# Kernel tuning notes

Hardware: AMD Instinct MI355X
Metric: run time of the kernel (lower is better)

## Reference

```python
import jax, jax.numpy as jnp
import numpy as np

N = 100_000   # nodes
E = 1_000_000 # edges
F = 128       # nfeat
H = 2         # heads
C = 64        # nhid (per-head out channels)
NEG_SLOPE = 0.2
BN_EPS = 1e-5


def setup_inputs() -> dict:
    key = jax.random.key(0)
    ks = jax.random.split(key, 6)
    x = jax.random.normal(ks[0], (N, F), dtype=jnp.float32)
    edge_index = jax.random.randint(ks[1], (2, E), 0, N, dtype=jnp.int32)
    # GATConv params (xavier-ish scale)
    W = jax.random.normal(ks[2], (F, H * C), dtype=jnp.float32) * np.float32(1.0 / np.sqrt(F))
    att_src = jax.random.normal(ks[3], (H, C), dtype=jnp.float32) * np.float32(0.1)
    att_dst = jax.random.normal(ks[4], (H, C), dtype=jnp.float32) * np.float32(0.1)
    bias = jnp.zeros((H * C,), dtype=jnp.float32)
    # BatchNorm1d affine params
    gamma = jnp.ones((H * C,), dtype=jnp.float32)
    beta = jnp.zeros((H * C,), dtype=jnp.float32)
    return {"x": x, "edge_index": edge_index, "W": W, "att_src": att_src,
            "att_dst": att_dst, "bias": bias, "gamma": gamma, "beta": beta}


def reference(x, edge_index, W, att_src, att_dst, bias, gamma, beta):
    n = x.shape[0]
    # --- GATConv (PyG semantics): add self-loops, per-head linear, edge attention ---
    loop = jnp.arange(n, dtype=edge_index.dtype)
    src = jnp.concatenate([edge_index[0], loop])  # message sources (j)
    dst = jnp.concatenate([edge_index[1], loop])  # aggregation targets (i)

    h = (x @ W).reshape(n, H, C)                      # [N,H,C]
    a_src = jnp.einsum('nhc,hc->nh', h, att_src)      # [N,H]
    a_dst = jnp.einsum('nhc,hc->nh', h, att_dst)      # [N,H]

    e = jax.nn.leaky_relu(a_src[src] + a_dst[dst], NEG_SLOPE)  # [Et,H]
    # segment softmax over incoming edges of each dst node
    m = jax.lax.stop_gradient(jax.ops.segment_max(e, dst, num_segments=n))
    e = jnp.exp(e - m[dst])
    s = jax.ops.segment_sum(e, dst, num_segments=n)
    alpha = e / s[dst]                                 # [Et,H]

    out = jax.ops.segment_sum(alpha[:, :, None] * h[src], dst, num_segments=n)  # [N,H,C]
    out = out.reshape(n, H * C) + bias                 # concat heads + bias

    # --- transition: ReLU -> BatchNorm1d (training-mode batch stats) -> Dropout(eval=identity) ---
    out = jax.nn.relu(out)
    mean = out.mean(axis=0)
    var = out.var(axis=0)  # biased, as BN uses for normalization
    out = gamma * (out - mean) * jax.lax.rsqrt(var + BN_EPS) + beta
    return out
```

## Files before the change

### kernel.cpp

```cpp
#include <hip/hip_runtime.h>

#define NN 100000
#define EE 1000000
#define ET (EE + NN)
#define HC 128
#define NB 391
#define AGG_BLOCKS 2048
#define NGRP (NN / 4)
#define NTILE 6250

typedef __attribute__((ext_vector_type(8))) short short8;
typedef __attribute__((ext_vector_type(4))) float f32x4;

__device__ __forceinline__ unsigned bfpack(float a, float b) {
    unsigned ua = __float_as_uint(a), ub = __float_as_uint(b);
    ua += 0x7fff + ((ua >> 16) & 1);
    ub += 0x7fff + ((ub >> 16) & 1);
    return (ua >> 16) | (ub & 0xffff0000u);
}

__global__ __launch_bounds__(64) void k_wprep(const float* __restrict__ W,
                                              uint4* __restrict__ wf)
{
    const int bid = blockIdx.x;
    const int ks = bid >> 3, nt = bid & 7;
    const int l = threadIdx.x;
    const int n = nt * 16 + (l & 15);
    const int k0 = ks * 32 + (l >> 4) * 8;
    unsigned u[4];
    #pragma unroll
    for (int r = 0; r < 4; ++r)
        u[r] = bfpack(W[(k0 + 2*r) * HC + n], W[(k0 + 2*r + 1) * HC + n]);
    wf[bid * 64 + l] = make_uint4(u[0], u[1], u[2], u[3]);
}

__global__ __launch_bounds__(256) void k_gemm(
    const float* __restrict__ x, const uint4* __restrict__ wf,
    const float* __restrict__ atts, const float* __restrict__ attd,
    unsigned* __restrict__ hB, float2* __restrict__ asrc2, float2* __restrict__ adst2)
{
    __shared__ uint4 wl[2048];
    for (int i = threadIdx.x; i < 2048; i += 256) wl[i] = wf[i];
    __syncthreads();

    const int wv = threadIdx.x >> 6, lane = threadIdx.x & 63;
    const int g = lane >> 4, c15 = lane & 15;

    float As[8], Ad[8];
    #pragma unroll
    for (int nt = 0; nt < 8; ++nt) {
        As[nt] = atts[nt * 16 + c15];
        Ad[nt] = attd[nt * 16 + c15];
    }

    for (int t = blockIdx.x * 4 + wv; t < NTILE; t += gridDim.x * 4) {
        const int row0 = t * 16;
        union { unsigned u[4]; short8 v; } af[4];
        const float* xr = x + (size_t)(row0 + c15) * HC + g * 8;
        #pragma unroll
        for (int ks = 0; ks < 4; ++ks) {
            float4 lo = *(const float4*)(xr + ks * 32);
            float4 hi = *(const float4*)(xr + ks * 32 + 4);
            af[ks].u[0] = bfpack(lo.x, lo.y);
            af[ks].u[1] = bfpack(lo.z, lo.w);
            af[ks].u[2] = bfpack(hi.x, hi.y);
            af[ks].u[3] = bfpack(hi.z, hi.w);
        }
        f32x4 acc[8];
        #pragma unroll
        for (int nt = 0; nt < 8; ++nt) acc[nt] = (f32x4)(0.f);
        #pragma unroll
        for (int nt = 0; nt < 8; ++nt) {
            #pragma unroll
            for (int ks = 0; ks < 4; ++ks) {
                short8 bfr = *(const short8*)&wl[(ks * 8 + nt) * 64 + lane];
                acc[nt] = __builtin_amdgcn_mfma_f32_16x16x32_bf16(
                    af[ks].v, bfr, acc[nt], 0, 0, 0);
            }
        }
        #pragma unroll
        for (int r = 0; r < 4; ++r) {
            const int row = row0 + g * 4 + r;
            float ps = 0.f, pd = 0.f, qs = 0.f, qd = 0.f;
            #pragma unroll
            for (int nt = 0; nt < 4; ++nt) {
                float a = acc[nt][r], b = acc[nt + 4][r];
                hB[(size_t)row * 64 + nt * 16 + c15] = bfpack(a, b);
                ps += a * As[nt];     qs += a * Ad[nt];
                pd += b * As[nt + 4]; qd += b * Ad[nt + 4];
            }
            for (int off = 8; off; off >>= 1) {
                ps += __shfl_xor(ps, off); pd += __shfl_xor(pd, off);
                qs += __shfl_xor(qs, off); qd += __shfl_xor(qd, off);
            }
            if (c15 == 0) {
                asrc2[row] = make_float2(ps, pd);
                adst2[row] = make_float2(qs, qd);
            }
        }
    }
}

__device__ __forceinline__ void edge_sd(const int* __restrict__ ei, int t, int& s, int& d) {
    if (t < EE) { s = ei[t]; d = ei[EE + t]; }
    else        { s = t - EE; d = t - EE; }
}

__global__ __launch_bounds__(256) void k_hist(const int* __restrict__ ei,
                                              int* __restrict__ hist)
{
    int t = blockIdx.x * 256 + threadIdx.x;
    if (t >= ET) return;
    int d = (t < EE) ? ei[EE + t] : (t - EE);
    atomicAdd(&hist[d], 1);
}

__global__ __launch_bounds__(256) void k_scan1(const int* __restrict__ hist,
                                               int* __restrict__ part)
{
    __shared__ int ls[256];
    int i = blockIdx.x * 256 + threadIdx.x;
    ls[threadIdx.x] = (i < NN) ? hist[i] : 0;
    __syncthreads();
    for (int off = 128; off; off >>= 1) {
        if (threadIdx.x < off) ls[threadIdx.x] += ls[threadIdx.x + off];
        __syncthreads();
    }
    if (!threadIdx.x) part[blockIdx.x] = ls[0];
}

__global__ __launch_bounds__(512) void k_scan2(int* __restrict__ part)
{
    __shared__ int ls[512];
    int tid = threadIdx.x;
    int v = (tid < NB) ? part[tid] : 0;
    ls[tid] = v;
    __syncthreads();
    for (int off = 1; off < 512; off <<= 1) {
        int t = (tid >= off) ? ls[tid - off] : 0;
        __syncthreads();
        ls[tid] += t;
        __syncthreads();
    }
    if (tid < NB) part[tid] = ls[tid] - v;
}

__global__ __launch_bounds__(256) void k_scan3(const int* __restrict__ hist,
                                               const int* __restrict__ part,
                                               int* __restrict__ row_ptr)
{
    __shared__ int ls[256];
    int i = blockIdx.x * 256 + threadIdx.x;
    int v = (i < NN) ? hist[i] : 0;
    ls[threadIdx.x] = v;
    __syncthreads();
    for (int off = 1; off < 256; off <<= 1) {
        int t = (threadIdx.x >= off) ? ls[threadIdx.x - off] : 0;
        __syncthreads();
        ls[threadIdx.x] += t;
        __syncthreads();
    }
    if (i < NN) row_ptr[i] = part[blockIdx.x] + ls[threadIdx.x] - v;
    if (i == 0) row_ptr[NN] = ET;
}

__global__ __launch_bounds__(256) void k_bucket(
    const int* __restrict__ ei, const int* __restrict__ row_ptr,
    int* __restrict__ cursor, int* __restrict__ csr_src)
{
    int t = blockIdx.x * 256 + threadIdx.x;
    if (t >= ET) return;
    int s, d; edge_sd(ei, t, s, d);
    int pos = row_ptr[d] + atomicAdd(&cursor[d], 1);
    csr_src[pos] = s;
}

__device__ __forceinline__ void gather8x2(const unsigned* base, const unsigned* off,
                                          unsigned long long* w) {
    asm volatile(
        "global_load_dwordx2 %0, %8,  %16\n\t"
        "global_load_dwordx2 %1, %9,  %16\n\t"
        "global_load_dwordx2 %2, %10, %16\n\t"
        "global_load_dwordx2 %3, %11, %16\n\t"
        "global_load_dwordx2 %4, %12, %16\n\t"
        "global_load_dwordx2 %5, %13, %16\n\t"
        "global_load_dwordx2 %6, %14, %16\n\t"
        "global_load_dwordx2 %7, %15, %16\n\t"
        "s_waitcnt vmcnt(0)"
        : "=&v"(w[0]), "=&v"(w[1]), "=&v"(w[2]), "=&v"(w[3]),
          "=&v"(w[4]), "=&v"(w[5]), "=&v"(w[6]), "=&v"(w[7])
        : "v"(off[0]), "v"(off[1]), "v"(off[2]), "v"(off[3]),
          "v"(off[4]), "v"(off[5]), "v"(off[6]), "v"(off[7]),
          "s"(base)
        : "memory");
}

__global__ __launch_bounds__(256) void k_agg(
    const int* __restrict__ row_ptr, const int* __restrict__ csr_src,
    const float2* __restrict__ asrc2, const float2* __restrict__ adst2,
    const unsigned* __restrict__ hB, const float* __restrict__ bias,
    float* __restrict__ out, float* __restrict__ bpart)
{
    __shared__ float lsum[HC], lsq[HC];
    __shared__ int    lidx[4][64];
    __shared__ float2 lp[4][64];
    const int tid = threadIdx.x;
    if (tid < HC) { lsum[tid] = 0.f; lsq[tid] = 0.f; }
    __syncthreads();

    const int wv = tid >> 6, lane = tid & 63;
    const int half = lane >> 5, m = lane & 31;
    const float bA0 = bias[2*m],      bB0 = bias[2*m + 1];
    const float bA1 = bias[2*m + 64], bB1 = bias[2*m + 65];

    for (int g = blockIdx.x; g < NGRP; g += AGG_BLOCKS) {
        const int node = g * 4 + wv;
        const int beg = row_ptr[node], end = row_ptr[node + 1];
        const float2 ad = adst2[node];

        float s0 = 0.f, s1 = 0.f;
        float a0 = 0.f, a1 = 0.f, b0 = 0.f, b1 = 0.f;

        for (int base = beg; base < end; base += 64) {
            const int cnt = min(64, end - base);
            if (lane < cnt) {
                int s = csr_src[base + lane];
                float2 av = asrc2[s];
                float e0 = av.x + ad.x; e0 = e0 > 0.f ? e0 : 0.2f * e0;
                float e1 = av.y + ad.y; e1 = e1 > 0.f ? e1 : 0.2f * e1;
                float2 pv = make_float2(__expf(e0), __expf(e1));
                lidx[wv][lane] = s;
                lp[wv][lane] = pv;
                s0 += pv.x; s1 += pv.y;
            }
            for (int j0 = 0; j0 < cnt; j0 += 16) {
                unsigned off[8]; unsigned long long w[8];
                float px[8], py[8];
                #pragma unroll
                for (int u = 0; u < 8; ++u) {
                    int j  = j0 + 2 * u + half;
                    int jc = j < cnt ? j : cnt - 1;
                    int s  = lidx[wv][jc];
                    float2 pv = lp[wv][jc];
                    px[u] = j < cnt ? pv.x : 0.f;
                    py[u] = j < cnt ? pv.y : 0.f;
                    off[u] = ((unsigned)s * 64u + (unsigned)m * 2u) * 4u;
                }
                gather8x2(hB, off, w);
                #pragma unroll
                for (int u = 0; u < 8; ++u) {
                    unsigned wlo = (unsigned)w[u];
                    unsigned whi = (unsigned)(w[u] >> 32);
                    a0 = fmaf(px[u], __uint_as_float(wlo << 16),          a0);
                    a1 = fmaf(py[u], __uint_as_float(wlo & 0xffff0000u),  a1);
                    b0 = fmaf(px[u], __uint_as_float(whi << 16),          b0);
                    b1 = fmaf(py[u], __uint_as_float(whi & 0xffff0000u),  b1);
                }
            }
        }

        a0 += __shfl_xor(a0, 32); a1 += __shfl_xor(a1, 32);
        b0 += __shfl_xor(b0, 32); b1 += __shfl_xor(b1, 32);
        for (int o = 32; o; o >>= 1) {
            s0 += __shfl_xor(s0, o);
            s1 += __shfl_xor(s1, o);
        }
        const float i0 = 1.f / s0, i1 = 1.f / s1;

        if (half == 0) {
            float vA0 = a0 * i0 + bA0; vA0 = vA0 > 0.f ? vA0 : 0.f;
            float vB0 = b0 * i0 + bB0; vB0 = vB0 > 0.f ? vB0 : 0.f;
            float vA1 = a1 * i1 + bA1; vA1 = vA1 > 0.f ? vA1 : 0.f;
            float vB1 = b1 * i1 + bB1; vB1 = vB1 > 0.f ? vB1 : 0.f;
            *(float2*)&out[(size_t)node * HC + 2*m]      = make_float2(vA0, vB0);
            *(float2*)&out[(size_t)node * HC + 64 + 2*m] = make_float2(vA1, vB1);
            atomicAdd(&lsum[2*m],      vA0); atomicAdd(&lsq[2*m],      vA0 * vA0);
            atomicAdd(&lsum[2*m + 1],  vB0); atomicAdd(&lsq[2*m + 1],  vB0 * vB0);
            atomicAdd(&lsum[2*m + 64], vA1); atomicAdd(&lsq[2*m + 64], vA1 * vA1);
            atomicAdd(&lsum[2*m + 65], vB1); atomicAdd(&lsq[2*m + 65], vB1 * vB1);
        }
    }

    __syncthreads();
    bpart[(size_t)blockIdx.x * 256 + tid] = tid < HC ? lsum[tid] : lsq[tid - HC];
}

__global__ __launch_bounds__(256) void k_red(const float* __restrict__ bpart,
                                             float* __restrict__ p2)
{
    const int tid = threadIdx.x;
    float acc = 0.f;
    const int r0 = blockIdx.x * (AGG_BLOCKS / 16);
    #pragma unroll 4
    for (int r = 0; r < AGG_BLOCKS / 16; ++r)
        acc += bpart[(size_t)(r0 + r) * 256 + tid];
    p2[blockIdx.x * 256 + tid] = acc;
}

__global__ void k_bnparam(const float* __restrict__ p2,
                          const float* __restrict__ gamma, const float* __restrict__ beta,
                          float* __restrict__ scsh)
{
    int c = threadIdx.x;
    float sum = 0.f, sq = 0.f;
    #pragma unroll
    for (int i = 0; i < 16; ++i) {
        sum += p2[i * 256 + c];
        sq  += p2[i * 256 + c + 128];
    }
    float mean = sum * (1.f / NN);
    float var  = sq * (1.f / NN) - mean * mean;
    float sc   = gamma[c] * rsqrtf(var + 1e-5f);
    scsh[c]       = sc;
    scsh[128 + c] = beta[c] - mean * sc;
}

__global__ __launch_bounds__(256) void k_apply(float* __restrict__ out,
                                               const float* __restrict__ scsh)
{
    size_t i = (size_t)blockIdx.x * 256 + threadIdx.x;
    if (i * 4 >= (size_t)NN * HC) return;
    float4 v = ((float4*)out)[i];
    int c = (int)((i * 4) & (HC - 1));
    v.x = v.x * scsh[c]     + scsh[128 + c];
    v.y = v.y * scsh[c + 1] + scsh[128 + c + 1];
    v.z = v.z * scsh[c + 2] + scsh[128 + c + 2];
    v.w = v.w * scsh[c + 3] + scsh[128 + c + 3];
    ((float4*)out)[i] = v;
}

extern "C" void kernel_launch(void* const* d_in, const int* in_sizes, int n_in,
                              void* d_out, int out_size, void* d_ws, size_t ws_size,
                              hipStream_t stream) {
    const float* x     = (const float*)d_in[0];
    const int*   ei    = (const int*)  d_in[1];
    const float* W     = (const float*)d_in[2];
    const float* atts  = (const float*)d_in[3];
    const float* attd  = (const float*)d_in[4];
    const float* bias  = (const float*)d_in[5];
    const float* gamma = (const float*)d_in[6];
    const float* beta  = (const float*)d_in[7];
    float* out = (float*)d_out;
    float* ws  = (float*)d_ws;

    unsigned* hB     = (unsigned*)ws;
    float*    asrc   = ws + 6400000;
    float*    adst   = ws + 6600000;
    int*      hist   = (int*)(ws + 6800000);
    int*      cursor = (int*)(ws + 6900000);
    float*    scsh   = ws + 7000256;
    int*      row_ptr= (int*)(ws + 7000512);
    int*      part   = (int*)(ws + 7100513);
    int*      csr_src= (int*)(ws + 7101025);
    float*    bpart  = ws + 10401026;
    float*    p2     = ws + 10925314;
    uint4*    wf     = (uint4*)(ws + 10929412);

    hipMemsetAsync(hist, 0, (size_t)200000 * sizeof(int), stream);

    k_wprep <<<32, 64, 0, stream>>>(W, wf);
    k_gemm  <<<782, 256, 0, stream>>>(x, wf, atts, attd, hB,
                                      (float2*)asrc, (float2*)adst);
    k_hist  <<<(ET + 255) / 256, 256, 0, stream>>>(ei, hist);
    k_scan1 <<<NB, 256, 0, stream>>>(hist, part);
    k_scan2 <<<1, 512, 0, stream>>>(part);
    k_scan3 <<<NB, 256, 0, stream>>>(hist, part, row_ptr);
    k_bucket<<<(ET + 255) / 256, 256, 0, stream>>>(ei, row_ptr, cursor, csr_src);
    k_agg   <<<AGG_BLOCKS, 256, 0, stream>>>(row_ptr, csr_src,
                                             (const float2*)asrc, (const float2*)adst,
                                             hB, bias, out, bpart);
    k_red   <<<16, 256, 0, stream>>>(bpart, p2);
    k_bnparam<<<1, 128, 0, stream>>>(p2, gamma, beta, scsh);
    k_apply <<<(NN * HC / 4 + 255) / 256, 256, 0, stream>>>(out, scsh);
}
```

Baseline: 340.1 us.

## Fuse histogram into GEMM kernel and precompute edge exponentials during bucketing

Merges the destination-histogram pass into the GEMM launch by giving 256 extra blocks the atomic counting work, so both run concurrently and one launch is saved. Moves the attention logit, leaky-ReLU and exp computation from the aggregation kernel into the bucketing kernel, which writes per-edge exp values in CSR order. Aggregation then reads them contiguously instead of gathering asrc by source index, and it gains an occupancy hint. The cost is an extra 8.8 MB written and read for pexp, plus random asrc/adst reads in the bucket pass.

```diff
diff --git a/kernel.cpp b/kernel.cpp
--- a/kernel.cpp
+++ b/kernel.cpp
@@ -8,6 +8,7 @@
 #define AGG_BLOCKS 2048
 #define NGRP (NN / 4)
 #define NTILE 6250
+#define GEMM_BLKS 768
 
 typedef __attribute__((ext_vector_type(8))) short short8;
 typedef __attribute__((ext_vector_type(4))) float f32x4;
@@ -34,12 +35,23 @@
     wf[bid * 64 + l] = make_uint4(u[0], u[1], u[2], u[3]);
 }
 
-__global__ __launch_bounds__(256) void k_gemm(
+__global__ __launch_bounds__(256) void k_gemmhist(
     const float* __restrict__ x, const uint4* __restrict__ wf,
     const float* __restrict__ atts, const float* __restrict__ attd,
-    unsigned* __restrict__ hB, float2* __restrict__ asrc2, float2* __restrict__ adst2)
+    unsigned* __restrict__ hB, float2* __restrict__ asrc2, float2* __restrict__ adst2,
+    const int* __restrict__ ei, int* __restrict__ hist)
 {
     __shared__ uint4 wl[2048];
+
+    if (blockIdx.x >= GEMM_BLKS) {
+        const int t0 = (blockIdx.x - GEMM_BLKS) * 256 + threadIdx.x;
+        for (int t = t0; t < ET; t += 256 * 256) {
+            int d = (t < EE) ? ei[EE + t] : (t - EE);
+            atomicAdd(&hist[d], 1);
+        }
+        return;
+    }
+
     for (int i = threadIdx.x; i < 2048; i += 256) wl[i] = wf[i];
     __syncthreads();
 
@@ -53,7 +65,7 @@
         Ad[nt] = attd[nt * 16 + c15];
     }
 
-    for (int t = blockIdx.x * 4 + wv; t < NTILE; t += gridDim.x * 4) {
+    for (int t = blockIdx.x * 4 + wv; t < NTILE; t += GEMM_BLKS * 4) {
         const int row0 = t * 16;
         union { unsigned u[4]; short8 v; } af[4];
         const float* xr = x + (size_t)(row0 + c15) * HC + g * 8;
@@ -106,15 +118,6 @@
     else        { s = t - EE; d = t - EE; }
 }
 
-__global__ __launch_bounds__(256) void k_hist(const int* __restrict__ ei,
-                                              int* __restrict__ hist)
-{
-    int t = blockIdx.x * 256 + threadIdx.x;
-    if (t >= ET) return;
-    int d = (t < EE) ? ei[EE + t] : (t - EE);
-    atomicAdd(&hist[d], 1);
-}
-
 __global__ __launch_bounds__(256) void k_scan1(const int* __restrict__ hist,
                                                int* __restrict__ part)
 {
@@ -165,14 +168,20 @@
 }
 
 __global__ __launch_bounds__(256) void k_bucket(
-    const int* __restrict__ ei, const int* __restrict__ row_ptr,
-    int* __restrict__ cursor, int* __restrict__ csr_src)
+    const int* __restrict__ ei, const float* __restrict__ asrc,
+    const float* __restrict__ adst, const int* __restrict__ row_ptr,
+    int* __restrict__ cursor, int* __restrict__ csr_src, float2* __restrict__ pexp)
 {
     int t = blockIdx.x * 256 + threadIdx.x;
     if (t >= ET) return;
     int s, d; edge_sd(ei, t, s, d);
+    float2 av = *(const float2*)&asrc[s * 2];
+    float2 dv = *(const float2*)&adst[d * 2];
+    float e0 = av.x + dv.x; e0 = e0 > 0.f ? e0 : 0.2f * e0;
+    float e1 = av.y + dv.y; e1 = e1 > 0.f ? e1 : 0.2f * e1;
     int pos = row_ptr[d] + atomicAdd(&cursor[d], 1);
     csr_src[pos] = s;
+    pexp[pos] = make_float2(__expf(e0), __expf(e1));
 }
 
 __device__ __forceinline__ void gather8x2(const unsigned* base, const unsigned* off,
@@ -195,10 +204,10 @@
         : "memory");
 }
 
-__global__ __launch_bounds__(256) void k_agg(
+__global__ __launch_bounds__(256, 8) void k_agg(
     const int* __restrict__ row_ptr, const int* __restrict__ csr_src,
-    const float2* __restrict__ asrc2, const float2* __restrict__ adst2,
-    const unsigned* __restrict__ hB, const float* __restrict__ bias,
+    const float2* __restrict__ pexp, const unsigned* __restrict__ hB,
+    const float* __restrict__ bias,
     float* __restrict__ out, float* __restrict__ bpart)
 {
     __shared__ float lsum[HC], lsq[HC];
@@ -216,7 +225,6 @@
     for (int g = blockIdx.x; g < NGRP; g += AGG_BLOCKS) {
         const int node = g * 4 + wv;
         const int beg = row_ptr[node], end = row_ptr[node + 1];
-        const float2 ad = adst2[node];
 
         float s0 = 0.f, s1 = 0.f;
         float a0 = 0.f, a1 = 0.f, b0 = 0.f, b1 = 0.f;
@@ -224,12 +232,8 @@
         for (int base = beg; base < end; base += 64) {
             const int cnt = min(64, end - base);
             if (lane < cnt) {
-                int s = csr_src[base + lane];
-                float2 av = asrc2[s];
-                float e0 = av.x + ad.x; e0 = e0 > 0.f ? e0 : 0.2f * e0;
-                float e1 = av.y + ad.y; e1 = e1 > 0.f ? e1 : 0.2f * e1;
-                float2 pv = make_float2(__expf(e0), __expf(e1));
-                lidx[wv][lane] = s;
+                float2 pv = pexp[base + lane];
+                lidx[wv][lane] = csr_src[base + lane];
                 lp[wv][lane] = pv;
                 s0 += pv.x; s1 += pv.y;
             }
@@ -352,24 +356,24 @@
     int*      row_ptr= (int*)(ws + 7000512);
     int*      part   = (int*)(ws + 7100513);
     int*      csr_src= (int*)(ws + 7101025);
+    float2*   pexp   = (float2*)(ws + 8201026);
     float*    bpart  = ws + 10401026;
     float*    p2     = ws + 10925314;
     uint4*    wf     = (uint4*)(ws + 10929412);
 
     hipMemsetAsync(hist, 0, (size_t)200000 * sizeof(int), stream);
 
-    k_wprep <<<32, 64, 0, stream>>>(W, wf);
-    k_gemm  <<<782, 256, 0, stream>>>(x, wf, atts, attd, hB,
-                                      (float2*)asrc, (float2*)adst);
-    k_hist  <<<(ET + 255) / 256, 256, 0, stream>>>(ei, hist);
-    k_scan1 <<<NB, 256, 0, stream>>>(hist, part);
-    k_scan2 <<<1, 512, 0, stream>>>(part);
-    k_scan3 <<<NB, 256, 0, stream>>>(hist, part, row_ptr);
-    k_bucket<<<(ET + 255) / 256, 256, 0, stream>>>(ei, row_ptr, cursor, csr_src);
-    k_agg   <<<AGG_BLOCKS, 256, 0, stream>>>(row_ptr, csr_src,
-                                             (const float2*)asrc, (const float2*)adst,
-                                             hB, bias, out, bpart);
-    k_red   <<<16, 256, 0, stream>>>(bpart, p2);
-    k_bnparam<<<1, 128, 0, stream>>>(p2, gamma, beta, scsh);
-    k_apply <<<(NN * HC / 4 + 255) / 256, 256, 0, stream>>>(out, scsh);
-}
+    k_wprep   <<<32, 64, 0, stream>>>(W, wf);
+    k_gemmhist<<<1024, 256, 0, stream>>>(x, wf, atts, attd, hB,
+                                         (float2*)asrc, (float2*)adst, ei, hist);
+    k_scan1   <<<NB, 256, 0, stream>>>(hist, part);
+    k_scan2   <<<1, 512, 0, stream>>>(part);
+    k_scan3   <<<NB, 256, 0, stream>>>(hist, part, row_ptr);
+    k_bucket  <<<(ET + 255) / 256, 256, 0, stream>>>(ei, asrc, adst, row_ptr,
+                                                     cursor, csr_src, pexp);
+    k_agg     <<<AGG_BLOCKS, 256, 0, stream>>>(row_ptr, csr_src, pexp, hB, bias,
+                                               out, bpart);
+    k_red     <<<16, 256, 0, stream>>>(bpart, p2);
+    k_bnparam <<<1, 128, 0, stream>>>(p2, gamma, beta, scsh);
+    k_apply   <<<(NN * HC / 4 + 255) / 256, 256, 0, stream>>>(out, scsh);
+}
```

Result: faster. 322.6 us (-5.2%).
